# Optimization experiments

Measured on AMD Instinct MI355X. Metric: run time of the kernel, lower is better.

Reference implementation:

```python
import jax, jax.numpy as jnp
import numpy as np
from jax.scipy.special import digamma, gammaln

COEF = 0.01
PRIOR = 1.0
IGNORE_INDEX = 255


def setup_inputs() -> dict:
    key = jax.random.key(0)
    k1, k2 = jax.random.split(key)
    pred = jax.random.normal(k1, (8, 19, 512, 512), dtype=jnp.float32)
    target = jax.random.randint(k2, (8, 512, 512), 0, 19, dtype=jnp.int64)
    return {"pred": pred, "target": target}


def reference(pred, target):
    # pred: [B, C, H, W] logits; target: [B, H, W] int class ids
    alphas = jnp.exp(pred)
    mask_ignore = target == IGNORE_INDEX
    tgt = jnp.where(mask_ignore, 0, target)
    # gather alpha at the answer class: [B, H, W]
    a_ans = jnp.take_along_axis(alphas, tgt[:, None, :, :], axis=1)[:, 0]
    a_zero = jnp.sum(alphas, axis=1)  # [B, H, W]
    ll_loss = digamma(a_ans) - digamma(a_zero)
    loss1 = gammaln(a_zero) - jnp.sum(gammaln(alphas), axis=1)
    loss2 = jnp.sum((alphas - PRIOR) * (digamma(alphas) - digamma(a_zero)[:, None, :, :]), axis=1)
    kl_loss = loss1 + loss2
    loss = COEF * kl_loss - ll_loss  # [B, H, W]
    loss = jnp.where(mask_ignore, jnp.zeros_like(loss), loss)
    avg_factor = jnp.sum(target != IGNORE_INDEX).astype(loss.dtype)
    return jnp.sum(loss) / avg_factor
```

## Files before the change

### kernel.cpp

```cpp
#include <hip/hip_runtime.h>


#define NCLS 19
#define HW (512 * 512)
#define NPIX (8 * HW)
#define IGNORE_IDX 255
#define COEF 0.01f

__device__ __forceinline__ float fast_rcp(float x) {
    return __builtin_amdgcn_rcpf(x);
}

__device__ __forceinline__ void dg_lg(float a, float& dg, float& lg) {
    float x1 = a + 1.f, x2 = a + 2.f, x3 = a + 3.f, x4 = a + 4.f, x5 = a + 5.f;
    float p = a * x1 * x2 * x3 * x4 * x5;
    float rsum = fast_rcp(a) + fast_rcp(x1) + fast_rcp(x2) +
                 fast_rcp(x3) + fast_rcp(x4) + fast_rcp(x5);
    float y = a + 6.f;
    float r = fast_rcp(y);
    float r2 = r * r;
    float ln_y = __logf(y);
    dg = ln_y - 0.5f * r
         - r2 * (0.0833333333f - r2 * (0.0083333333f - r2 * 0.0039682540f))
         - rsum;
    lg = (y - 0.5f) * ln_y - y + 0.91893853320467f
         + r * (0.0833333333f - r2 * (0.0027777778f - r2 * 0.00079365079f))
         - __logf(p);
}

__global__ __launch_bounds__(256) void bml_main(const float* __restrict__ pred,
                                                const int* __restrict__ target,
                                                double* __restrict__ ws) {
    int tid = blockIdx.x * blockDim.x + threadIdx.x;
    int nth = gridDim.x * blockDim.x;

    float local = 0.f;
    unsigned cnt = 0;

    for (int p = tid; p < NPIX; p += nth) {
        int b = p >> 18;
        int hw = p & (HW - 1);
        const float* base = pred + (size_t)b * NCLS * HW + hw;

        int t = target[p];
        bool ignore = (t == IGNORE_IDX);
        int tc = ignore ? 0 : t;

        float a0 = 0.f, slg = 0.f, s2 = 0.f, dg_ans = 0.f;
        #pragma unroll
        for (int c = 0; c < NCLS; ++c) {
            float a = __expf(base[(size_t)c * HW]);
            float dg, lg;
            dg_lg(a, dg, lg);
            a0 += a;
            slg += lg;
            s2 += (a - 1.f) * dg;
            if (c == tc) dg_ans = dg;
        }
        float dg0, lg0;
        dg_lg(a0, dg0, lg0);

        float ll = dg_ans - dg0;
        float loss1 = lg0 - slg;
        float loss2 = s2 - dg0 * (a0 - (float)NCLS);
        float loss = COEF * (loss1 + loss2) - ll;

        if (!ignore) { local += loss; cnt++; }
    }

    #pragma unroll
    for (int off = 32; off; off >>= 1) {
        local += __shfl_down(local, off);
        cnt   += __shfl_down(cnt, off);
    }
    __shared__ float s_sum[4];
    __shared__ unsigned s_cnt[4];
    int lane = threadIdx.x & 63, wid = threadIdx.x >> 6;
    if (lane == 0) { s_sum[wid] = local; s_cnt[wid] = cnt; }
    __syncthreads();
    if (threadIdx.x == 0) {
        float bs = s_sum[0] + s_sum[1] + s_sum[2] + s_sum[3];
        unsigned bc = s_cnt[0] + s_cnt[1] + s_cnt[2] + s_cnt[3];
        atomicAdd(&ws[0], (double)bs);
        atomicAdd(&ws[1], (double)bc);
    }
}

__global__ void bml_finalize(const double* __restrict__ ws, float* __restrict__ out) {
    if (threadIdx.x == 0 && blockIdx.x == 0)
        out[0] = (float)(ws[0] / ws[1]);
}

extern "C" void kernel_launch(void* const* d_in, const int* in_sizes, int n_in,
                              void* d_out, int out_size, void* d_ws, size_t ws_size,
                              hipStream_t stream) {
    const float* pred = (const float*)d_in[0];
    const int* target = (const int*)d_in[1];
    float* out = (float*)d_out;
    double* ws = (double*)d_ws;

    hipMemsetAsync(d_ws, 0, 2 * sizeof(double), stream);

    const int block = 256;
    const int grid = 2048;
    bml_main<<<grid, block, 0, stream>>>(pred, target, ws);
    bml_finalize<<<1, 64, 0, stream>>>(ws, out);
}
```

Baseline: 270.9 us.

## Cut per-channel digamma/lgamma cost and vectorize four pixels per thread

Measured after the change: 263.0 us. 2.9% less time.

```diff
diff --git a/kernel.cpp b/kernel.cpp
--- a/kernel.cpp
+++ b/kernel.cpp
@@ -5,68 +5,105 @@
 #define HW (512 * 512)
 #define NPIX (8 * HW)
 #define IGNORE_IDX 255
-#define COEF 0.01f
 
-__device__ __forceinline__ float fast_rcp(float x) {
-    return __builtin_amdgcn_rcpf(x);
+#define PC1 0.08333333333f
+#define PC2 0.00833333333f
+#define PC3 0.00396825397f
+#define GL1 0.08333333333f
+#define GL2 0.00277777778f
+#define GL3 0.00079365079f
+#define HLN2PI 0.918938533205f
+#define LN2F 0.693147180560f
+
+__device__ __forceinline__ float fast_rcp(float x) { return __builtin_amdgcn_rcpf(x); }
+
+struct Acc {
+    float a0, s2, slgy, dgans;
+    double ppd;
+};
+
+__device__ __forceinline__ void chan(float x, int c, int tc, Acc& A) {
+    float a  = __expf(x);
+    float a1 = a + 1.f, a2 = a + 2.f, y = a + 3.f;
+    float p  = a * a1 * a2;
+    float rpy = fast_rcp(p * y);
+    float r  = p * rpy;
+    float rp = y * rpy;
+    float q  = __fmaf_rn(a, __fmaf_rn(a, 3.f, 6.f), 2.f);
+    float ly = __logf(y);
+    float r2 = r * r;
+    float psiy = ly - 0.5f * r - r2 * (PC1 - r2 * (PC2 - r2 * PC3));
+    float psia = psiy - q * rp;
+    A.s2 = __fmaf_rn(a - 1.f, psia, A.s2);
+    A.a0 += a;
+    float lgy = __fmaf_rn(y - 0.5f, ly, -y) + HLN2PI
+                + r * (GL1 - r2 * (GL2 - r2 * GL3));
+    A.slgy += lgy;
+    A.ppd *= (double)p;
+    A.dgans = (c == tc) ? psia : A.dgans;
 }
 
-__device__ __forceinline__ void dg_lg(float a, float& dg, float& lg) {
-    float x1 = a + 1.f, x2 = a + 2.f, x3 = a + 3.f, x4 = a + 4.f, x5 = a + 5.f;
-    float p = a * x1 * x2 * x3 * x4 * x5;
-    float rsum = fast_rcp(a) + fast_rcp(x1) + fast_rcp(x2) +
-                 fast_rcp(x3) + fast_rcp(x4) + fast_rcp(x5);
-    float y = a + 6.f;
-    float r = fast_rcp(y);
+__device__ __forceinline__ float finish(const Acc& A) {
+    float a0 = A.a0;
+    float a1 = a0 + 1.f, a2 = a0 + 2.f, y = a0 + 3.f;
+    float p  = a0 * a1 * a2;
+    float rpy = fast_rcp(p * y);
+    float r  = p * rpy, rp = y * rpy;
+    float q  = __fmaf_rn(a0, __fmaf_rn(a0, 3.f, 6.f), 2.f);
+    float ly = __logf(y);
     float r2 = r * r;
-    float ln_y = __logf(y);
-    dg = ln_y - 0.5f * r
-         - r2 * (0.0833333333f - r2 * (0.0083333333f - r2 * 0.0039682540f))
-         - rsum;
-    lg = (y - 0.5f) * ln_y - y + 0.91893853320467f
-         + r * (0.0833333333f - r2 * (0.0027777778f - r2 * 0.00079365079f))
-         - __logf(p);
+    float psi0 = ly - 0.5f * r - r2 * (PC1 - r2 * (PC2 - r2 * PC3)) - q * rp;
+    float lg0  = __fmaf_rn(y - 0.5f, ly, -y) + HLN2PI
+                 + r * (GL1 - r2 * (GL2 - r2 * GL3)) - __logf(p);
+    int hi = __double2hiint(A.ppd);
+    int lo = __double2loint(A.ppd);
+    int e  = ((hi >> 20) & 0x7FF) - 1023;
+    double mant = __hiloint2double((hi & 0x000FFFFF) | 0x3FF00000, lo);
+    float lnpp = __logf((float)mant) + (float)e * LN2F;
+
+    float ll    = A.dgans - psi0;
+    float loss1 = lg0 - (A.slgy - lnpp);
+    float loss2 = A.s2 - psi0 * (a0 - (float)NCLS);
+    return 0.01f * (loss1 + loss2) - ll;
 }
 
 __global__ __launch_bounds__(256) void bml_main(const float* __restrict__ pred,
                                                 const int* __restrict__ target,
                                                 double* __restrict__ ws) {
-    int tid = blockIdx.x * blockDim.x + threadIdx.x;
-    int nth = gridDim.x * blockDim.x;
+    int g  = blockIdx.x * blockDim.x + threadIdx.x;
+    int p4 = g << 2;
+    int b  = p4 >> 18;
+    int hw = p4 & (HW - 1);
+    const float4* base = (const float4*)(pred + (size_t)b * NCLS * HW + hw);
+
+    int4 t4 = *(const int4*)(target + p4);
+    int tc0 = (t4.x == IGNORE_IDX) ? 0 : t4.x;
+    int tc1 = (t4.y == IGNORE_IDX) ? 0 : t4.y;
+    int tc2 = (t4.z == IGNORE_IDX) ? 0 : t4.z;
+    int tc3 = (t4.w == IGNORE_IDX) ? 0 : t4.w;
+
+    Acc A0 = {0.f, 0.f, 0.f, 0.f, 1.0};
+    Acc A1 = {0.f, 0.f, 0.f, 0.f, 1.0};
+    Acc A2 = {0.f, 0.f, 0.f, 0.f, 1.0};
+    Acc A3 = {0.f, 0.f, 0.f, 0.f, 1.0};
+
+    #pragma unroll 2
+    for (int c = 0; c < NCLS; ++c) {
+        float4 x = base[(size_t)c * (HW / 4)];
+        chan(x.x, c, tc0, A0);
+        chan(x.y, c, tc1, A1);
+        chan(x.z, c, tc2, A2);
+        chan(x.w, c, tc3, A3);
+    }
+
+    float l0 = finish(A0), l1 = finish(A1), l2 = finish(A2), l3 = finish(A3);
 
     float local = 0.f;
     unsigned cnt = 0;
-
-    for (int p = tid; p < NPIX; p += nth) {
-        int b = p >> 18;
-        int hw = p & (HW - 1);
-        const float* base = pred + (size_t)b * NCLS * HW + hw;
-
-        int t = target[p];
-        bool ignore = (t == IGNORE_IDX);
-        int tc = ignore ? 0 : t;
-
-        float a0 = 0.f, slg = 0.f, s2 = 0.f, dg_ans = 0.f;
-        #pragma unroll
-        for (int c = 0; c < NCLS; ++c) {
-            float a = __expf(base[(size_t)c * HW]);
-            float dg, lg;
-            dg_lg(a, dg, lg);
-            a0 += a;
-            slg += lg;
-            s2 += (a - 1.f) * dg;
-            if (c == tc) dg_ans = dg;
-        }
-        float dg0, lg0;
-        dg_lg(a0, dg0, lg0);
-
-        float ll = dg_ans - dg0;
-        float loss1 = lg0 - slg;
-        float loss2 = s2 - dg0 * (a0 - (float)NCLS);
-        float loss = COEF * (loss1 + loss2) - ll;
-
-        if (!ignore) { local += loss; cnt++; }
-    }
+    if (t4.x != IGNORE_IDX) { local += l0; cnt++; }
+    if (t4.y != IGNORE_IDX) { local += l1; cnt++; }
+    if (t4.z != IGNORE_IDX) { local += l2; cnt++; }
+    if (t4.w != IGNORE_IDX) { local += l3; cnt++; }
 
     #pragma unroll
     for (int off = 32; off; off >>= 1) {
@@ -102,7 +139,7 @@
     hipMemsetAsync(d_ws, 0, 2 * sizeof(double), stream);
 
     const int block = 256;
-    const int grid = 2048;
+    const int grid = NPIX / (block * 4);
     bml_main<<<grid, block, 0, stream>>>(pred, target, ws);
     bml_finalize<<<1, 64, 0, stream>>>(ws, out);
 }
```
